# Kernel tuning notes

Hardware: AMD Instinct MI355X
Metric: run time of the kernel (lower is better)

The kernel has to match this reference:

```python
import jax, jax.numpy as jnp
import numpy as np

# static sizes
B, N_PER, D, H, L, DFF, IN_DIM = 32, 1024, 128, 4, 3, 2048, 64
N = B * N_PER
HD = D // H
EPS = 1e-5


def setup_inputs() -> dict:
    key = jax.random.key(0)
    ks = jax.random.split(key, 16)
    s = 0.02
    rn = lambda k, shp: jax.random.normal(k, shp, jnp.float32) * s
    return {
        "x": jax.random.normal(ks[0], (N, IN_DIM), jnp.float32),
        # uniform graph sizes -> static max_nodes; sorted graph ids
        "batch": jnp.repeat(jnp.arange(B, dtype=jnp.int32), N_PER),
        "W_in": rn(ks[1], (D, IN_DIM)),
        "b_in": rn(ks[2], (D,)),
        "Wqkv": rn(ks[3], (L, 3 * D, D)),
        "bqkv": rn(ks[4], (L, 3 * D)),
        "Wo": rn(ks[5], (L, D, D)),
        "bo": rn(ks[6], (L, D)),
        "W1": rn(ks[7], (L, DFF, D)),
        "b1": rn(ks[8], (L, DFF)),
        "W2": rn(ks[9], (L, D, DFF)),
        "b2": rn(ks[10], (L, D)),
        "ln1_g": jnp.ones((L, D), jnp.float32),
        "ln1_b": jnp.zeros((L, D), jnp.float32),
        "ln2_g": jnp.ones((L, D), jnp.float32),
        "ln2_b": jnp.zeros((L, D), jnp.float32),
    }


def _ln(x, g, b):
    m = x.mean(-1, keepdims=True)
    v = jnp.mean((x - m) ** 2, axis=-1, keepdims=True)
    return (x - m) / jnp.sqrt(v + EPS) * g + b


def _mha(h, Wqkv, bqkv, Wo, bo):
    # h: [B, S, D]
    qkv = h @ Wqkv.T + bqkv                      # [B, S, 3D]
    q, k, v = jnp.split(qkv, 3, axis=-1)
    q = q.reshape(B, -1, H, HD)
    k = k.reshape(B, -1, H, HD)
    v = v.reshape(B, -1, H, HD)
    att = jnp.einsum("bqhd,bkhd->bhqk", q, k) / np.sqrt(HD).astype(np.float32)
    p = jax.nn.softmax(att, axis=-1)
    o = jnp.einsum("bhqk,bkhd->bqhd", p, v).reshape(B, -1, D)
    return o @ Wo.T + bo


def reference(x, batch, W_in, b_in, Wqkv, bqkv, Wo, bo, W1, b1, W2, b2,
              ln1_g, ln1_b, ln2_g, ln2_b):
    # fused ragged -> padded: project all nodes once, scatter by (graph, pos)
    h = x @ W_in.T + b_in                        # [N, D]
    starts = jnp.searchsorted(batch, jnp.arange(B, dtype=batch.dtype))
    pos = jnp.arange(N, dtype=batch.dtype) - starts[batch]
    padded = jnp.zeros((B, N_PER, D), h.dtype).at[batch, pos].set(h)

    out = padded
    for l in range(L):  # post-LN TransformerEncoderLayer, dropout=eval
        a = _mha(out, Wqkv[l], bqkv[l], Wo[l], bo[l])
        out = _ln(out + a, ln1_g[l], ln1_b[l])
        f = jax.nn.relu(out @ W1[l].T + b1[l]) @ W2[l].T + b2[l]
        out = _ln(out + f, ln2_g[l], ln2_b[l])

    # mask derived from projected inputs, exactly as the original
    mask = (padded.sum(axis=2) != 0).astype(out.dtype)  # [B, S]
    return (out * mask[:, :, None]).sum(axis=1) / mask.sum(axis=1, keepdims=True)
```

## Files before the change

kernel.cpp:

```cpp
#include <hip/hip_runtime.h>
#include <hip/hip_bf16.h>
#include <stdint.h>

#define BB    32
#define NPER  1024
#define NTOT  32768
#define DD    128
#define HH    4
#define HD    32
#define LL    3
#define DFF   2048
#define INDIM 64
#define QKSCALE 0.17677669529663687f

typedef unsigned short u16;
typedef short bf16x8 __attribute__((ext_vector_type(8)));
typedef float f32x4 __attribute__((ext_vector_type(4)));

#define AS_GLOBAL(p) ((const __attribute__((address_space(1))) void*)(p))
#define AS_LDS(p)    ((__attribute__((address_space(3))) void*)(p))

__device__ __forceinline__ float bf2f(u16 v){
  unsigned u = ((unsigned)v) << 16; float f; __builtin_memcpy(&f, &u, 4); return f;
}
__device__ __forceinline__ u16 f2bf(float f){
  unsigned u; __builtin_memcpy(&u, &f, 4);
  unsigned lsb = (u >> 16) & 1u;
  u += 0x7fffu + lsb;
  return (u16)(u >> 16);
}

constexpr size_t OFF_FLAG   = 0;
constexpr size_t OFF_STARTS = 256;
constexpr size_t OFF_BIN    = 1024;
constexpr size_t OFF_BQKV   = OFF_BIN   + 128*4;
constexpr size_t OFF_BO     = OFF_BQKV  + 1152*4;
constexpr size_t OFF_B1     = OFF_BO    + 384*4;
constexpr size_t OFF_B2     = OFF_B1    + 6144*4;
constexpr size_t OFF_LN1G   = OFF_B2    + 384*4;
constexpr size_t OFF_LN1B   = OFF_LN1G  + 384*4;
constexpr size_t OFF_LN2G   = OFF_LN1B  + 384*4;
constexpr size_t OFF_LN2B   = OFF_LN2G  + 384*4;
constexpr size_t OFF_XB     = 40960;
constexpr size_t OFF_WINB   = OFF_XB    + (size_t)2097152*2;
constexpr size_t OFF_WQKVB  = OFF_WINB  + (size_t)8192*2;
constexpr size_t OFF_WOB    = OFF_WQKVB + (size_t)147456*2;
constexpr size_t OFF_W1B    = OFF_WOB   + (size_t)49152*2;
constexpr size_t OFF_W2B    = OFF_W1B   + (size_t)786432*2;
constexpr size_t OFF_CUR    = OFF_W2B   + (size_t)786432*2;
constexpr size_t OFF_TMP    = OFF_CUR   + (size_t)4194304*4;
constexpr size_t OFF_CURB   = OFF_TMP   + (size_t)4194304*4;
constexpr size_t OFF_QKVB   = OFF_CURB  + (size_t)4194304*2;
constexpr size_t OFF_ATTNOB = OFF_QKVB  + (size_t)12582912*2;
constexpr size_t OFF_ACTB   = OFF_ATTNOB+ (size_t)4194304*2;
constexpr size_t OFF_MASK   = OFF_ACTB  + (size_t)16777216*2;
constexpr size_t OFF_VT     = OFF_MASK  + (size_t)NTOT*4;
constexpr size_t OFF_RED    = OFF_VT    + (size_t)4096*1024*2;
constexpr size_t OFF_CNT    = OFF_RED   + (size_t)32*8*128*4;

__device__ __forceinline__ int plaus(unsigned bits){
  if ((bits << 1) == 0u) return 1;
  unsigned e = (bits >> 23) & 0xFFu;
  return (e >= 100u && e <= 140u) ? 1 : 0;
}
__global__ void detect_kernel(const unsigned* __restrict__ x, int* __restrict__ flag){
  __shared__ int red[256];
  int t = threadIdx.x, c = 0;
  for (int i = t; i < 2048; i += 256){
    unsigned w = x[i];
    c += (plaus(w << 16) & plaus(w & 0xFFFF0000u));
  }
  red[t] = c; __syncthreads();
  for (int s = 128; s > 0; s >>= 1){ if (t < s) red[t] += red[t+s]; __syncthreads(); }
  if (t == 0) *flag = (red[0] >= 1229) ? 1 : 0;
}

__global__ void starts_kernel(const int* __restrict__ batch, int* __restrict__ starts){
  int b = threadIdx.x;
  if (b < BB){
    int lo = 0, hi = NTOT;
    while (lo < hi){ int mid = (lo + hi) >> 1; if (batch[mid] < b) lo = mid + 1; else hi = mid; }
    starts[b] = lo;
  }
}

struct ConvSeg { const void* src; void* dst; int n; int tobf; };
struct ConvArgs { ConvSeg s[15]; };

__global__ __launch_bounds__(256) void convall_kernel(ConvArgs a, const int* __restrict__ flag){
  const int isb = *flag;
  const int blk = blockIdx.x;
  int seg = -1, base = 0, lb = 0;
  #pragma unroll
  for (int i = 0; i < 15; ++i){
    int nb = (a.s[i].n + 1023) >> 10;
    if (seg < 0){
      if (blk < base + nb){ seg = i; lb = blk - base; }
      base += nb;
    }
  }
  const ConvSeg sg = a.s[seg];
  const int idx = lb*1024 + threadIdx.x*4;
  if (idx >= sg.n) return;
  if (sg.tobf){
    u16* dst = (u16*)sg.dst + idx;
    if (isb){
      *(uint2*)dst = *(const uint2*)((const u16*)sg.src + idx);
    } else {
      const float* s4 = (const float*)sg.src + idx;
      dst[0] = f2bf(s4[0]); dst[1] = f2bf(s4[1]);
      dst[2] = f2bf(s4[2]); dst[3] = f2bf(s4[3]);
    }
  } else {
    float* dst = (float*)sg.dst + idx;
    if (isb){
      const u16* s4 = (const u16*)sg.src + idx;
      dst[0] = bf2f(s4[0]); dst[1] = bf2f(s4[1]);
      dst[2] = bf2f(s4[2]); dst[3] = bf2f(s4[3]);
    } else {
      *(float4*)dst = *(const float4*)((const float*)sg.src + idx);
    }
  }
}

__global__ __launch_bounds__(256) void gemm_bf16(
    const u16* __restrict__ A, int lda,
    const u16* __restrict__ W, int ldw,
    const float* __restrict__ bias,
    float* __restrict__ Cf, u16* __restrict__ Cb,
    int N, int K, int flags)
{
  __shared__ __align__(16) u16 At[64][32];
  __shared__ __align__(16) u16 Wt[64][32];
  const int t = threadIdx.x;
  const int m0 = blockIdx.x * 64, n0 = blockIdx.y * 64;
  const int wave = t >> 6, lane = t & 63;
  const int quad = lane >> 4, l16 = lane & 15;
  const int lr = t >> 2, lc = (t & 3) * 8;

  f32x4 acc[4];
  #pragma unroll
  for (int i = 0; i < 4; ++i){ acc[i][0]=0.f; acc[i][1]=0.f; acc[i][2]=0.f; acc[i][3]=0.f; }

  const u16* Arow = A + (size_t)(m0 + lr) * lda + lc;
  const u16* Wrow = W + (size_t)(n0 + lr) * ldw + lc;

  for (int k0 = 0; k0 < K; k0 += 32){
    uint4 av = *(const uint4*)(Arow + k0);
    uint4 wv = *(const uint4*)(Wrow + k0);
    __syncthreads();
    *(uint4*)&At[lr][lc] = av;
    *(uint4*)&Wt[lr][lc] = wv;
    __syncthreads();
    bf16x8 af = *(const bf16x8*)&At[wave*16 + l16][quad*8];
    #pragma unroll
    for (int nt = 0; nt < 4; ++nt){
      bf16x8 wf = *(const bf16x8*)&Wt[nt*16 + l16][quad*8];
      acc[nt] = __builtin_amdgcn_mfma_f32_16x16x32_bf16(af, wf, acc[nt], 0, 0, 0);
    }
  }
  const int row = m0 + wave*16 + quad*4;
  #pragma unroll
  for (int nt = 0; nt < 4; ++nt){
    const int col = n0 + nt*16 + l16;
    const float bv = bias ? bias[col] : 0.f;
    #pragma unroll
    for (int r = 0; r < 4; ++r){
      size_t idx = (size_t)(row + r) * N + col;
      float v = acc[nt][r] + bv;
      if (flags & 1) v = fmaxf(v, 0.f);
      if (Cf) Cf[idx] = v;
      if (Cb) Cb[idx] = f2bf(v);
    }
  }
}

__global__ __launch_bounds__(128) void scatter_kernel(
    const float* __restrict__ hlin, const int* __restrict__ batch,
    const int* __restrict__ starts, float* __restrict__ cur,
    u16* __restrict__ curb, float* __restrict__ mask)
{
  int i = blockIdx.x, t = threadIdx.x;
  int g = batch[i];
  int p = i - starts[g];
  float v = hlin[(size_t)i*DD + t];
  float s = v;
  #pragma unroll
  for (int off = 32; off; off >>= 1) s += __shfl_xor(s, off);
  __shared__ float sh[2];
  if ((t & 63) == 0) sh[t >> 6] = s;
  __syncthreads();
  float rowsum = sh[0] + sh[1];
  if ((unsigned)p < (unsigned)NPER && (unsigned)g < (unsigned)BB){
    size_t j = (size_t)g*NPER + p;
    cur[j*DD + t]  = v;
    curb[j*DD + t] = f2bf(v);
    if (t == 0) mask[j] = (rowsum != 0.f) ? 1.f : 0.f;
  }
}

__global__ __launch_bounds__(256) void fattn_kernel(
    const u16* __restrict__ qkvb,
    const u16* __restrict__ vt,
    u16* __restrict__ attnob)
{
  __shared__ __align__(16) u16 Klds[2][2048];
  __shared__ __align__(16) u16 Vl[2][2048];
  __shared__ __align__(16) u16 Pl[4][2][16*72];

  const int t = threadIdx.x;
  const int wave = t >> 6, lane = t & 63;
  const int quad = lane >> 4, l16 = lane & 15;
  const int q0 = blockIdx.x * 128;
  const int h = blockIdx.y, b = blockIdx.z;
  const size_t qkvbase = (size_t)b * NPER * 384;
  const u16* Kg = qkvb + qkvbase + 128 + h*HD;
  const u16* Vg = vt + (size_t)((b*HH + h)*HD) * NPER;

  bf16x8 qf[2];
  #pragma unroll
  for (int qt = 0; qt < 2; ++qt){
    const u16* qp = qkvb + qkvbase + (size_t)(q0 + wave*32 + qt*16 + l16)*384 + h*HD + quad*8;
    uint4 qv = *(const uint4*)qp;
    u16 raw[8]; __builtin_memcpy(raw, &qv, 16);
    #pragma unroll
    for (int j = 0; j < 8; ++j) qf[qt][j] = (short)f2bf(bf2f(raw[j]) * QKSCALE);
  }

  const int vcv = wave*2 + (lane >> 5), vd = lane & 31;
  auto stage = [&](int buf, int kt){
    __builtin_amdgcn_global_load_lds(
        AS_GLOBAL(Kg + (size_t)(kt*64 + lane)*384 + wave*8),
        AS_LDS(&Klds[buf][wave*64*8]), 16, 0, 0);
    __builtin_amdgcn_global_load_lds(
        AS_GLOBAL(Vg + (size_t)vd*NPER + kt*64 + vcv*8),
        AS_LDS(&Vl[buf][wave*64*8]), 16, 0, 0);
  };

  float lsum[2] = {0.f, 0.f};
  f32x4 o[2][2];
  #pragma unroll
  for (int qt = 0; qt < 2; ++qt)
    #pragma unroll
    for (int i = 0; i < 2; ++i){ o[qt][i][0]=0.f; o[qt][i][1]=0.f; o[qt][i][2]=0.f; o[qt][i][3]=0.f; }

  stage(0, 0);
  asm volatile("s_waitcnt vmcnt(0)" ::: "memory");
  __syncthreads();

  for (int kt = 0; kt < 16; ++kt){
    const int buf = kt & 1;
    if (kt + 1 < 16) stage(buf ^ 1, kt + 1);

    f32x4 sfr[2][4];
    #pragma unroll
    for (int nt = 0; nt < 4; ++nt){
      bf16x8 kf = *(const bf16x8*)&Klds[buf][(quad*64 + nt*16 + l16)*8];
      f32x4 z = {0.f,0.f,0.f,0.f};
      sfr[0][nt] = __builtin_amdgcn_mfma_f32_16x16x32_bf16(kf, qf[0], z, 0, 0, 0);
      sfr[1][nt] = __builtin_amdgcn_mfma_f32_16x16x32_bf16(kf, qf[1], z, 0, 0, 0);
    }

    #pragma unroll
    for (int qt = 0; qt < 2; ++qt){
      float ps = 0.f;
      #pragma unroll
      for (int nt = 0; nt < 4; ++nt){
        float e0 = __expf(sfr[qt][nt][0]), e1 = __expf(sfr[qt][nt][1]);
        float e2 = __expf(sfr[qt][nt][2]), e3 = __expf(sfr[qt][nt][3]);
        ps += (e0 + e1) + (e2 + e3);
        uint2 w;
        w.x = (unsigned)f2bf(e0) | ((unsigned)f2bf(e1) << 16);
        w.y = (unsigned)f2bf(e2) | ((unsigned)f2bf(e3) << 16);
        *(uint2*)&Pl[wave][qt][l16*72 + nt*16 + quad*4] = w;
      }
      ps += __shfl_xor(ps, 16);
      ps += __shfl_xor(ps, 32);
      lsum[qt] += ps;
    }
    asm volatile("s_waitcnt lgkmcnt(0)" ::: "memory");

    #pragma unroll
    for (int kk = 0; kk < 2; ++kk){
      bf16x8 v0 = *(const bf16x8*)&Vl[buf][((kk*4 + quad)*32 + l16)*8];
      bf16x8 v1 = *(const bf16x8*)&Vl[buf][((kk*4 + quad)*32 + 16 + l16)*8];
      #pragma unroll
      for (int qt = 0; qt < 2; ++qt){
        bf16x8 pf = *(const bf16x8*)&Pl[wave][qt][l16*72 + kk*32 + quad*8];
        o[qt][0] = __builtin_amdgcn_mfma_f32_16x16x32_bf16(pf, v0, o[qt][0], 0, 0, 0);
        o[qt][1] = __builtin_amdgcn_mfma_f32_16x16x32_bf16(pf, v1, o[qt][1], 0, 0, 0);
      }
    }

    if (kt + 1 < 16){
      asm volatile("s_waitcnt vmcnt(0)" ::: "memory");
      __syncthreads();
    }
  }

  #pragma unroll
  for (int qt = 0; qt < 2; ++qt){
    #pragma unroll
    for (int r = 0; r < 4; ++r){
      float inv = 1.f / __shfl(lsum[qt], quad*4 + r);
      int row = q0 + wave*32 + qt*16 + quad*4 + r;
      size_t base = (size_t)(b*NPER + row)*DD + h*HD;
      attnob[base + l16]      = f2bf(o[qt][0][r] * inv);
      attnob[base + 16 + l16] = f2bf(o[qt][1][r] * inv);
    }
  }
}

__device__ __forceinline__ void epilogue_ln64(
    const f32x4 O[8], int m0, int wave, int quad, int l16,
    const float* __restrict__ bias, const float* __restrict__ g,
    const float* __restrict__ beta, float* __restrict__ cur,
    u16* __restrict__ curb)
{
  #pragma unroll
  for (int rr = 0; rr < 4; ++rr){
    int row = m0 + wave*16 + quad*4 + rr;
    float vs[8], sum = 0.f;
    #pragma unroll
    for (int nt = 0; nt < 8; ++nt){
      int col = nt*16 + l16;
      float v = O[nt][rr] + bias[col] + cur[(size_t)row*DD + col];
      vs[nt] = v; sum += v;
    }
    sum += __shfl_xor(sum, 1); sum += __shfl_xor(sum, 2);
    sum += __shfl_xor(sum, 4); sum += __shfl_xor(sum, 8);
    float mean = sum * (1.f/DD);
    float sq = 0.f;
    #pragma unroll
    for (int nt = 0; nt < 8; ++nt){ float d = vs[nt] - mean; sq += d*d; }
    sq += __shfl_xor(sq, 1); sq += __shfl_xor(sq, 2);
    sq += __shfl_xor(sq, 4); sq += __shfl_xor(sq, 8);
    float rs = rsqrtf(sq * (1.f/DD) + 1e-5f);
    #pragma unroll
    for (int nt = 0; nt < 8; ++nt){
      int col = nt*16 + l16;
      float o = (vs[nt] - mean)*rs*g[col] + beta[col];
      cur[(size_t)row*DD + col]  = o;
      curb[(size_t)row*DD + col] = f2bf(o);
    }
  }
}

__global__ __launch_bounds__(256) void wgemm_kernel(
    const u16* __restrict__ A,
    const u16* __restrict__ Wbase,
    const float* __restrict__ biasb,
    int mode,
    u16* __restrict__ outb, int opitch,
    u16* __restrict__ vtout,
    float* __restrict__ cur, u16* __restrict__ curb,
    const float* __restrict__ g, const float* __restrict__ beta)
{
  __shared__ __align__(16) u16 Wl[16384];
  const int t = threadIdx.x, wave = t >> 6, lane = t & 63;
  const int quad = lane >> 4, l16 = lane & 15;
  const int m0 = blockIdx.x * 64, nb = blockIdx.y;
  const u16* Wsl = Wbase + (size_t)nb * 16384;
  const float* bias = biasb + nb * 128;

  #pragma unroll
  for (int j = 0; j < 8; ++j){
    int s = t + 256*j;
    int r = s >> 4, cx = (s & 15) ^ (r & 15);
    *(uint4*)&Wl[s*8] = *(const uint4*)(Wsl + (size_t)r*128 + cx*8);
  }
  bf16x8 af[4];
  #pragma unroll
  for (int kk = 0; kk < 4; ++kk)
    af[kk] = *(const bf16x8*)(A + (size_t)(m0 + wave*16 + l16)*128 + kk*32 + quad*8);
  __syncthreads();

  f32x4 O[8];
  #pragma unroll
  for (int nt = 0; nt < 8; ++nt){ O[nt][0]=0.f; O[nt][1]=0.f; O[nt][2]=0.f; O[nt][3]=0.f; }

  #pragma unroll
  for (int nt = 0; nt < 8; ++nt){
    int row = nt*16 + l16;
    bf16x8 wf[4];
    #pragma unroll
    for (int kk = 0; kk < 4; ++kk)
      wf[kk] = *(const bf16x8*)&Wl[(row*16 + ((kk*4 + quad) ^ l16))*8];
    #pragma unroll
    for (int kk = 0; kk < 4; ++kk)
      O[nt] = __builtin_amdgcn_mfma_f32_16x16x32_bf16(af[kk], wf[kk], O[nt], 0, 0, 0);
  }

  if (mode == 0){
    if (nb == 2 && vtout){
      int rowb = m0 + wave*16 + quad*4;
      int bg = rowb >> 10, s = rowb & 1023;
      #pragma unroll
      for (int nt = 0; nt < 8; ++nt){
        int col = nt*16 + l16;
        int hh = col >> 5, d = col & 31;
        float v0 = O[nt][0] + bias[col], v1 = O[nt][1] + bias[col];
        float v2 = O[nt][2] + bias[col], v3 = O[nt][3] + bias[col];
        uint2 w;
        w.x = (unsigned)f2bf(v0) | ((unsigned)f2bf(v1) << 16);
        w.y = (unsigned)f2bf(v2) | ((unsigned)f2bf(v3) << 16);
        *(uint2*)(vtout + (size_t)((bg*HH + hh)*HD + d)*NPER + s) = w;
      }
    } else {
      #pragma unroll
      for (int rr = 0; rr < 4; ++rr){
        int row = m0 + wave*16 + quad*4 + rr;
        #pragma unroll
        for (int nt = 0; nt < 8; ++nt){
          int col = nt*16 + l16;
          outb[(size_t)row*opitch + nb*128 + col] = f2bf(O[nt][rr] + bias[col]);
        }
      }
    }
  } else {
    epilogue_ln64(O, m0, wave, quad, l16, bias, g, beta, cur, curb);
  }
}

__global__ __launch_bounds__(256, 2) void ffn_kernel(
    const u16* __restrict__ Ag,
    const u16* __restrict__ W1g,
    const u16* __restrict__ W2g,
    const float* __restrict__ b1,
    const float* __restrict__ b2,
    const float* __restrict__ g, const float* __restrict__ beta,
    float* __restrict__ cur, u16* __restrict__ curb)
{
  __shared__ __align__(16) u16 W1l[2][8192];
  __shared__ __align__(16) u16 W2l[2][8192];
  __shared__ __align__(16) u16 Pl[4][16*72];

  const int t = threadIdx.x, wave = t >> 6, lane = t & 63;
  const int quad = lane >> 4, l16 = lane & 15;
  const int m0 = blockIdx.x * 64;
  u16* Pw = &Pl[wave][0];

  auto stage = [&](int buf, int dffc){
    #pragma unroll
    for (int i = 0; i < 4; ++i){
      const int s0 = wave*256 + i*64;
      const int s  = s0 + lane;
      { int r = s >> 4, cx = (s & 15) ^ (r & 15);
        __builtin_amdgcn_global_load_lds(
            AS_GLOBAL(W1g + (size_t)(dffc + r)*128 + cx*8),
            AS_LDS(&W1l[buf][s0*8]), 16, 0, 0); }
      { int r = s >> 3, cx = (s & 7) ^ (r & 7);
        __builtin_amdgcn_global_load_lds(
            AS_GLOBAL(W2g + (size_t)r*DFF + dffc + cx*8),
            AS_LDS(&W2l[buf][s0*8]), 16, 0, 0); }
    }
  };

  bf16x8 af[4];
  #pragma unroll
  for (int kk = 0; kk < 4; ++kk)
    af[kk] = *(const bf16x8*)(Ag + (size_t)(m0 + wave*16 + l16)*128 + kk*32 + quad*8);

  f32x4 O[8];
  #pragma unroll
  for (int nt = 0; nt < 8; ++nt){ O[nt][0]=0.f; O[nt][1]=0.f; O[nt][2]=0.f; O[nt][3]=0.f; }

  stage(0, 0);
  asm volatile("s_waitcnt vmcnt(0)" ::: "memory");
  __syncthreads();

  for (int c = 0; c < 32; ++c){
    const int buf = c & 1;
    if (c + 1 < 32) stage(buf ^ 1, (c + 1)*64);

    #pragma unroll
    for (int nt = 0; nt < 4; ++nt){
      int row = nt*16 + l16;
      bf16x8 wf[4];
      #pragma unroll
      for (int kk = 0; kk < 4; ++kk)
        wf[kk] = *(const bf16x8*)&W1l[buf][(row*16 + ((kk*4 + quad) ^ l16))*8];
      f32x4 b1v = *(const f32x4*)&b1[c*64 + nt*16 + quad*4];
      f32x4 s = {0.f,0.f,0.f,0.f};
      #pragma unroll
      for (int kk = 0; kk < 4; ++kk)
        s = __builtin_amdgcn_mfma_f32_16x16x32_bf16(wf[kk], af[kk], s, 0, 0, 0);
      float v0 = fmaxf(s[0] + b1v[0], 0.f), v1 = fmaxf(s[1] + b1v[1], 0.f);
      float v2 = fmaxf(s[2] + b1v[2], 0.f), v3 = fmaxf(s[3] + b1v[3], 0.f);
      uint2 w;
      w.x = (unsigned)f2bf(v0) | ((unsigned)f2bf(v1) << 16);
      w.y = (unsigned)f2bf(v2) | ((unsigned)f2bf(v3) << 16);
      *(uint2*)&Pw[l16*72 + nt*16 + quad*4] = w;
    }
    asm volatile("s_waitcnt lgkmcnt(0)" ::: "memory");

    bf16x8 pf[2];
    #pragma unroll
    for (int kk = 0; kk < 2; ++kk)
      pf[kk] = *(const bf16x8*)&Pw[l16*72 + kk*32 + quad*8];
    #pragma unroll
    for (int nt = 0; nt < 8; ++nt){
      int row = nt*16 + l16;
      bf16x8 wf[2];
      #pragma unroll
      for (int kk = 0; kk < 2; ++kk)
        wf[kk] = *(const bf16x8*)&W2l[buf][(row*8 + ((kk*4 + quad) ^ (l16 & 7)))*8];
      #pragma unroll
      for (int kk = 0; kk < 2; ++kk)
        O[nt] = __builtin_amdgcn_mfma_f32_16x16x32_bf16(pf[kk], wf[kk], O[nt], 0, 0, 0);
    }

    if (c + 1 < 32){
      asm volatile("s_waitcnt vmcnt(0)" ::: "memory");
      __syncthreads();
    }
  }

  epilogue_ln64(O, m0, wave, quad, l16, b2, g, beta, cur, curb);
}

__global__ __launch_bounds__(128) void reduce1_kernel(
    const float* __restrict__ cur, const float* __restrict__ mask,
    float* __restrict__ partial, float* __restrict__ cnt)
{
  int b = blockIdx.x, c = blockIdx.y, t = threadIdx.x;
  float acc = 0.f, cn = 0.f;
  for (int s = c*128; s < c*128 + 128; ++s){
    float mk = mask[b*NPER + s];
    acc += cur[(size_t)(b*NPER + s)*DD + t] * mk;
    cn += mk;
  }
  partial[(size_t)(b*8 + c)*DD + t] = acc;
  if (t == 0) cnt[b*8 + c] = cn;
}
__global__ __launch_bounds__(128) void reduce2_kernel(
    const float* __restrict__ partial, const float* __restrict__ cnt,
    const int* __restrict__ flag, void* __restrict__ out)
{
  int b = blockIdx.x, t = threadIdx.x;
  float acc = 0.f, cn = 0.f;
  #pragma unroll
  for (int c = 0; c < 8; ++c){
    acc += partial[(size_t)(b*8 + c)*DD + t];
    cn  += cnt[b*8 + c];
  }
  float val = acc / cn;
  if (*flag) ((u16*)out)[b*DD + t] = f2bf(val);
  else       ((float*)out)[b*DD + t] = val;
}

extern "C" void kernel_launch(void* const* d_in, const int* in_sizes, int n_in,
                              void* d_out, int out_size, void* d_ws, size_t ws_size,
                              hipStream_t stream)
{
  (void)in_sizes; (void)n_in; (void)out_size; (void)ws_size;
  char* ws = (char*)d_ws;
  int*   flag   = (int*)(ws + OFF_FLAG);
  int*   starts = (int*)(ws + OFF_STARTS);
  float* BIN  = (float*)(ws + OFF_BIN);
  float* BQKV = (float*)(ws + OFF_BQKV);
  float* BO   = (float*)(ws + OFF_BO);
  float* B1   = (float*)(ws + OFF_B1);
  float* B2   = (float*)(ws + OFF_B2);
  float* LN1G = (float*)(ws + OFF_LN1G);
  float* LN1B = (float*)(ws + OFF_LN1B);
  float* LN2G = (float*)(ws + OFF_LN2G);
  float* LN2B = (float*)(ws + OFF_LN2B);
  u16* XB    = (u16*)(ws + OFF_XB);
  u16* WINB  = (u16*)(ws + OFF_WINB);
  u16* WQKVB = (u16*)(ws + OFF_WQKVB);
  u16* WOB   = (u16*)(ws + OFF_WOB);
  u16* W1B   = (u16*)(ws + OFF_W1B);
  u16* W2B   = (u16*)(ws + OFF_W2B);
  float* CUR = (float*)(ws + OFF_CUR);
  float* TMP = (float*)(ws + OFF_TMP);
  u16* CURB  = (u16*)(ws + OFF_CURB);
  u16* QKVB  = (u16*)(ws + OFF_QKVB);
  u16* ATTNOB= (u16*)(ws + OFF_ATTNOB);
  float* MASK= (float*)(ws + OFF_MASK);
  u16* VT    = (u16*)(ws + OFF_VT);
  float* RED = (float*)(ws + OFF_RED);
  float* CNT = (float*)(ws + OFF_CNT);

  detect_kernel<<<1, 256, 0, stream>>>((const unsigned*)d_in[0], flag);
  starts_kernel<<<1, 64, 0, stream>>>((const int*)d_in[1], starts);

  ConvArgs ca;
  ca.s[0]  = { d_in[0],  XB,    NTOT*INDIM, 1 };
  ca.s[1]  = { d_in[2],  WINB,  DD*INDIM,   1 };
  ca.s[2]  = { d_in[4],  WQKVB, LL*3*DD*DD, 1 };
  ca.s[3]  = { d_in[6],  WOB,   LL*DD*DD,   1 };
  ca.s[4]  = { d_in[8],  W1B,   LL*DFF*DD,  1 };
  ca.s[5]  = { d_in[10], W2B,   LL*DD*DFF,  1 };
  ca.s[6]  = { d_in[3],  BIN,   DD,         0 };
  ca.s[7]  = { d_in[5],  BQKV,  LL*3*DD,    0 };
  ca.s[8]  = { d_in[7],  BO,    LL*DD,      0 };
  ca.s[9]  = { d_in[9],  B1,    LL*DFF,     0 };
  ca.s[10] = { d_in[11], B2,    LL*DD,      0 };
  ca.s[11] = { d_in[12], LN1G,  LL*DD,      0 };
  ca.s[12] = { d_in[13], LN1B,  LL*DD,      0 };
  ca.s[13] = { d_in[14], LN2G,  LL*DD,      0 };
  ca.s[14] = { d_in[15], LN2B,  LL*DD,      0 };
  int nblk = 0;
  for (int i = 0; i < 15; ++i) nblk += (ca.s[i].n + 1023) >> 10;
  convall_kernel<<<nblk, 256, 0, stream>>>(ca, flag);

  gemm_bf16<<<dim3(NTOT/64, DD/64), 256, 0, stream>>>(
      XB, INDIM, WINB, INDIM, BIN, TMP, nullptr, DD, INDIM, 0);
  scatter_kernel<<<NTOT, 128, 0, stream>>>(TMP, (const int*)d_in[1], starts, CUR, CURB, MASK);

  for (int l = 0; l < LL; ++l){
    wgemm_kernel<<<dim3(NTOT/64, 3), 256, 0, stream>>>(
        CURB, WQKVB + (size_t)l*3*DD*DD, BQKV + l*3*DD, 0,
        QKVB, 384, VT, nullptr, nullptr, nullptr, nullptr);
    fattn_kernel<<<dim3(NPER/128, HH, BB), 256, 0, stream>>>(QKVB, VT, ATTNOB);
    wgemm_kernel<<<dim3(NTOT/64, 1), 256, 0, stream>>>(
        ATTNOB, WOB + (size_t)l*DD*DD, BO + l*DD, 1,
        nullptr, 0, nullptr, CUR, CURB, LN1G + l*DD, LN1B + l*DD);
    ffn_kernel<<<dim3(NTOT/64), 256, 0, stream>>>(
        CURB, W1B + (size_t)l*DFF*DD, W2B + (size_t)l*DD*DFF,
        B1 + l*DFF, B2 + l*DD, LN2G + l*DD, LN2B + l*DD, CUR, CURB);
  }

  reduce1_kernel<<<dim3(BB, 8), 128, 0, stream>>>(CUR, MASK, RED, CNT);
  reduce2_kernel<<<BB, 128, 0, stream>>>(RED, CNT, flag, d_out);
}
```

Baseline: 507.8 us.

## Fuse input projection with scatter, widen QKV GEMM tile, restructure FFN P store

```diff
diff --git a/kernel.cpp b/kernel.cpp
--- a/kernel.cpp
+++ b/kernel.cpp
@@ -123,79 +123,69 @@
   }
 }
 
-__global__ __launch_bounds__(256) void gemm_bf16(
-    const u16* __restrict__ A, int lda,
-    const u16* __restrict__ W, int ldw,
-    const float* __restrict__ bias,
-    float* __restrict__ Cf, u16* __restrict__ Cb,
-    int N, int K, int flags)
-{
-  __shared__ __align__(16) u16 At[64][32];
-  __shared__ __align__(16) u16 Wt[64][32];
-  const int t = threadIdx.x;
-  const int m0 = blockIdx.x * 64, n0 = blockIdx.y * 64;
-  const int wave = t >> 6, lane = t & 63;
+__global__ __launch_bounds__(256) void inproj_kernel(
+    const u16* __restrict__ XB,
+    const u16* __restrict__ WINB,
+    const float* __restrict__ bin,
+    const int* __restrict__ batch, const int* __restrict__ starts,
+    float* __restrict__ cur, u16* __restrict__ curb, float* __restrict__ mask)
+{
+  __shared__ __align__(16) u16 Wl[8192];
+  const int t = threadIdx.x, wave = t >> 6, lane = t & 63;
   const int quad = lane >> 4, l16 = lane & 15;
-  const int lr = t >> 2, lc = (t & 3) * 8;
-
-  f32x4 acc[4];
-  #pragma unroll
-  for (int i = 0; i < 4; ++i){ acc[i][0]=0.f; acc[i][1]=0.f; acc[i][2]=0.f; acc[i][3]=0.f; }
-
-  const u16* Arow = A + (size_t)(m0 + lr) * lda + lc;
-  const u16* Wrow = W + (size_t)(n0 + lr) * ldw + lc;
-
-  for (int k0 = 0; k0 < K; k0 += 32){
-    uint4 av = *(const uint4*)(Arow + k0);
-    uint4 wv = *(const uint4*)(Wrow + k0);
-    __syncthreads();
-    *(uint4*)&At[lr][lc] = av;
-    *(uint4*)&Wt[lr][lc] = wv;
-    __syncthreads();
-    bf16x8 af = *(const bf16x8*)&At[wave*16 + l16][quad*8];
-    #pragma unroll
-    for (int nt = 0; nt < 4; ++nt){
-      bf16x8 wf = *(const bf16x8*)&Wt[nt*16 + l16][quad*8];
-      acc[nt] = __builtin_amdgcn_mfma_f32_16x16x32_bf16(af, wf, acc[nt], 0, 0, 0);
-    }
-  }
-  const int row = m0 + wave*16 + quad*4;
-  #pragma unroll
-  for (int nt = 0; nt < 4; ++nt){
-    const int col = n0 + nt*16 + l16;
-    const float bv = bias ? bias[col] : 0.f;
-    #pragma unroll
-    for (int r = 0; r < 4; ++r){
-      size_t idx = (size_t)(row + r) * N + col;
-      float v = acc[nt][r] + bv;
-      if (flags & 1) v = fmaxf(v, 0.f);
-      if (Cf) Cf[idx] = v;
-      if (Cb) Cb[idx] = f2bf(v);
-    }
-  }
-}
-
-__global__ __launch_bounds__(128) void scatter_kernel(
-    const float* __restrict__ hlin, const int* __restrict__ batch,
-    const int* __restrict__ starts, float* __restrict__ cur,
-    u16* __restrict__ curb, float* __restrict__ mask)
-{
-  int i = blockIdx.x, t = threadIdx.x;
-  int g = batch[i];
-  int p = i - starts[g];
-  float v = hlin[(size_t)i*DD + t];
-  float s = v;
-  #pragma unroll
-  for (int off = 32; off; off >>= 1) s += __shfl_xor(s, off);
-  __shared__ float sh[2];
-  if ((t & 63) == 0) sh[t >> 6] = s;
+  const int m0 = blockIdx.x * 64;
+
+  #pragma unroll
+  for (int j = 0; j < 4; ++j){
+    int s = t + 256*j;
+    int r = s >> 3, c8 = (s & 7) ^ (r & 7);
+    *(uint4*)&Wl[s*8] = *(const uint4*)(WINB + (size_t)r*INDIM + c8*8);
+  }
+  bf16x8 af[2];
+  #pragma unroll
+  for (int kk = 0; kk < 2; ++kk)
+    af[kk] = *(const bf16x8*)(XB + (size_t)(m0 + wave*16 + l16)*INDIM + kk*32 + quad*8);
   __syncthreads();
-  float rowsum = sh[0] + sh[1];
-  if ((unsigned)p < (unsigned)NPER && (unsigned)g < (unsigned)BB){
-    size_t j = (size_t)g*NPER + p;
-    cur[j*DD + t]  = v;
-    curb[j*DD + t] = f2bf(v);
-    if (t == 0) mask[j] = (rowsum != 0.f) ? 1.f : 0.f;
+
+  f32x4 O[8];
+  #pragma unroll
+  for (int nt = 0; nt < 8; ++nt){ O[nt][0]=0.f; O[nt][1]=0.f; O[nt][2]=0.f; O[nt][3]=0.f; }
+
+  #pragma unroll
+  for (int nt = 0; nt < 8; ++nt){
+    int row = nt*16 + l16;
+    bf16x8 wf[2];
+    #pragma unroll
+    for (int kk = 0; kk < 2; ++kk)
+      wf[kk] = *(const bf16x8*)&Wl[(row*8 + ((kk*4 + quad) ^ (row & 7)))*8];
+    #pragma unroll
+    for (int kk = 0; kk < 2; ++kk)
+      O[nt] = __builtin_amdgcn_mfma_f32_16x16x32_bf16(af[kk], wf[kk], O[nt], 0, 0, 0);
+  }
+
+  #pragma unroll
+  for (int rr = 0; rr < 4; ++rr){
+    int node = m0 + wave*16 + quad*4 + rr;
+    int gr = batch[node];
+    int p  = node - starts[gr];
+    float vs[8], sum = 0.f;
+    #pragma unroll
+    for (int nt = 0; nt < 8; ++nt){
+      float v = O[nt][rr] + bin[nt*16 + l16];
+      vs[nt] = v; sum += v;
+    }
+    sum += __shfl_xor(sum, 1); sum += __shfl_xor(sum, 2);
+    sum += __shfl_xor(sum, 4); sum += __shfl_xor(sum, 8);
+    if ((unsigned)p < (unsigned)NPER && (unsigned)gr < (unsigned)BB){
+      size_t j = (size_t)gr*NPER + p;
+      #pragma unroll
+      for (int nt = 0; nt < 8; ++nt){
+        int col = nt*16 + l16;
+        cur[j*DD + col]  = vs[nt];
+        curb[j*DD + col] = f2bf(vs[nt]);
+      }
+      if (l16 == 0) mask[j] = (sum != 0.f) ? 1.f : 0.f;
+    }
   }
 }
 
@@ -350,16 +340,56 @@
     const u16* __restrict__ A,
     const u16* __restrict__ Wbase,
     const float* __restrict__ biasb,
-    int mode,
-    u16* __restrict__ outb, int opitch,
-    u16* __restrict__ vtout,
     float* __restrict__ cur, u16* __restrict__ curb,
     const float* __restrict__ g, const float* __restrict__ beta)
 {
   __shared__ __align__(16) u16 Wl[16384];
   const int t = threadIdx.x, wave = t >> 6, lane = t & 63;
   const int quad = lane >> 4, l16 = lane & 15;
-  const int m0 = blockIdx.x * 64, nb = blockIdx.y;
+  const int m0 = blockIdx.x * 64;
+
+  #pragma unroll
+  for (int j = 0; j < 8; ++j){
+    int s = t + 256*j;
+    int r = s >> 4, cx = (s & 15) ^ (r & 15);
+    *(uint4*)&Wl[s*8] = *(const uint4*)(Wbase + (size_t)r*128 + cx*8);
+  }
+  bf16x8 af[4];
+  #pragma unroll
+  for (int kk = 0; kk < 4; ++kk)
+    af[kk] = *(const bf16x8*)(A + (size_t)(m0 + wave*16 + l16)*128 + kk*32 + quad*8);
+  __syncthreads();
+
+  f32x4 O[8];
+  #pragma unroll
+  for (int nt = 0; nt < 8; ++nt){ O[nt][0]=0.f; O[nt][1]=0.f; O[nt][2]=0.f; O[nt][3]=0.f; }
+
+  #pragma unroll
+  for (int nt = 0; nt < 8; ++nt){
+    int row = nt*16 + l16;
+    bf16x8 wf[4];
+    #pragma unroll
+    for (int kk = 0; kk < 4; ++kk)
+      wf[kk] = *(const bf16x8*)&Wl[(row*16 + ((kk*4 + quad) ^ l16))*8];
+    #pragma unroll
+    for (int kk = 0; kk < 4; ++kk)
+      O[nt] = __builtin_amdgcn_mfma_f32_16x16x32_bf16(af[kk], wf[kk], O[nt], 0, 0, 0);
+  }
+
+  epilogue_ln64(O, m0, wave, quad, l16, biasb, g, beta, cur, curb);
+}
+
+__global__ __launch_bounds__(256) void wgemm2_kernel(
+    const u16* __restrict__ A,
+    const u16* __restrict__ Wbase,
+    const float* __restrict__ biasb,
+    u16* __restrict__ outb, int opitch,
+    u16* __restrict__ vtout)
+{
+  __shared__ __align__(16) u16 Wl[16384];
+  const int t = threadIdx.x, wave = t >> 6, lane = t & 63;
+  const int quad = lane >> 4, l16 = lane & 15;
+  const int m0 = blockIdx.x * 128, nb = blockIdx.y;
   const u16* Wsl = Wbase + (size_t)nb * 16384;
   const float* bias = biasb + nb * 128;
 
@@ -369,15 +399,19 @@
     int r = s >> 4, cx = (s & 15) ^ (r & 15);
     *(uint4*)&Wl[s*8] = *(const uint4*)(Wsl + (size_t)r*128 + cx*8);
   }
-  bf16x8 af[4];
-  #pragma unroll
-  for (int kk = 0; kk < 4; ++kk)
-    af[kk] = *(const bf16x8*)(A + (size_t)(m0 + wave*16 + l16)*128 + kk*32 + quad*8);
+  bf16x8 af[2][4];
+  #pragma unroll
+  for (int mt = 0; mt < 2; ++mt)
+    #pragma unroll
+    for (int kk = 0; kk < 4; ++kk)
+      af[mt][kk] = *(const bf16x8*)(A + (size_t)(m0 + wave*32 + mt*16 + l16)*128 + kk*32 + quad*8);
   __syncthreads();
 
-  f32x4 O[8];
-  #pragma unroll
-  for (int nt = 0; nt < 8; ++nt){ O[nt][0]=0.f; O[nt][1]=0.f; O[nt][2]=0.f; O[nt][3]=0.f; }
+  f32x4 O[2][8];
+  #pragma unroll
+  for (int mt = 0; mt < 2; ++mt)
+    #pragma unroll
+    for (int nt = 0; nt < 8; ++nt){ O[mt][nt][0]=0.f; O[mt][nt][1]=0.f; O[mt][nt][2]=0.f; O[mt][nt][3]=0.f; }
 
   #pragma unroll
   for (int nt = 0; nt < 8; ++nt){
@@ -387,38 +421,41 @@
     for (int kk = 0; kk < 4; ++kk)
       wf[kk] = *(const bf16x8*)&Wl[(row*16 + ((kk*4 + quad) ^ l16))*8];
     #pragma unroll
-    for (int kk = 0; kk < 4; ++kk)
-      O[nt] = __builtin_amdgcn_mfma_f32_16x16x32_bf16(af[kk], wf[kk], O[nt], 0, 0, 0);
-  }
-
-  if (mode == 0){
-    if (nb == 2 && vtout){
-      int rowb = m0 + wave*16 + quad*4;
+    for (int mt = 0; mt < 2; ++mt)
+      #pragma unroll
+      for (int kk = 0; kk < 4; ++kk)
+        O[mt][nt] = __builtin_amdgcn_mfma_f32_16x16x32_bf16(af[mt][kk], wf[kk], O[mt][nt], 0, 0, 0);
+  }
+
+  if (nb == 2){
+    #pragma unroll
+    for (int mt = 0; mt < 2; ++mt){
+      int rowb = m0 + wave*32 + mt*16 + quad*4;
       int bg = rowb >> 10, s = rowb & 1023;
       #pragma unroll
       for (int nt = 0; nt < 8; ++nt){
         int col = nt*16 + l16;
         int hh = col >> 5, d = col & 31;
-        float v0 = O[nt][0] + bias[col], v1 = O[nt][1] + bias[col];
-        float v2 = O[nt][2] + bias[col], v3 = O[nt][3] + bias[col];
+        float v0 = O[mt][nt][0] + bias[col], v1 = O[mt][nt][1] + bias[col];
+        float v2 = O[mt][nt][2] + bias[col], v3 = O[mt][nt][3] + bias[col];
         uint2 w;
         w.x = (unsigned)f2bf(v0) | ((unsigned)f2bf(v1) << 16);
         w.y = (unsigned)f2bf(v2) | ((unsigned)f2bf(v3) << 16);
         *(uint2*)(vtout + (size_t)((bg*HH + hh)*HD + d)*NPER + s) = w;
       }
-    } else {
+    }
+  } else {
+    #pragma unroll
+    for (int mt = 0; mt < 2; ++mt)
       #pragma unroll
       for (int rr = 0; rr < 4; ++rr){
-        int row = m0 + wave*16 + quad*4 + rr;
+        int row = m0 + wave*32 + mt*16 + quad*4 + rr;
         #pragma unroll
         for (int nt = 0; nt < 8; ++nt){
           int col = nt*16 + l16;
-          outb[(size_t)row*opitch + nb*128 + col] = f2bf(O[nt][rr] + bias[col]);
+          outb[(size_t)row*opitch + nb*128 + col] = f2bf(O[mt][nt][rr] + bias[col]);
         }
       }
-    }
-  } else {
-    epilogue_ln64(O, m0, wave, quad, l16, bias, g, beta, cur, curb);
   }
 }
 
@@ -480,17 +517,14 @@
       #pragma unroll
       for (int kk = 0; kk < 4; ++kk)
         wf[kk] = *(const bf16x8*)&W1l[buf][(row*16 + ((kk*4 + quad) ^ l16))*8];
-      f32x4 b1v = *(const f32x4*)&b1[c*64 + nt*16 + quad*4];
+      float b1v = b1[c*64 + row];
       f32x4 s = {0.f,0.f,0.f,0.f};
       #pragma unroll
       for (int kk = 0; kk < 4; ++kk)
-        s = __builtin_amdgcn_mfma_f32_16x16x32_bf16(wf[kk], af[kk], s, 0, 0, 0);
-      float v0 = fmaxf(s[0] + b1v[0], 0.f), v1 = fmaxf(s[1] + b1v[1], 0.f);
-      float v2 = fmaxf(s[2] + b1v[2], 0.f), v3 = fmaxf(s[3] + b1v[3], 0.f);
-      uint2 w;
-      w.x = (unsigned)f2bf(v0) | ((unsigned)f2bf(v1) << 16);
-      w.y = (unsigned)f2bf(v2) | ((unsigned)f2bf(v3) << 16);
-      *(uint2*)&Pw[l16*72 + nt*16 + quad*4] = w;
+        s = __builtin_amdgcn_mfma_f32_16x16x32_bf16(af[kk], wf[kk], s, 0, 0, 0);
+      #pragma unroll
+      for (int rr = 0; rr < 4; ++rr)
+        Pw[(quad*4 + rr)*72 + nt*16 + l16] = f2bf(fmaxf(s[rr] + b1v, 0.f));
     }
     asm volatile("s_waitcnt lgkmcnt(0)" ::: "memory");
 
@@ -573,7 +607,6 @@
   u16* W1B   = (u16*)(ws + OFF_W1B);
   u16* W2B   = (u16*)(ws + OFF_W2B);
   float* CUR = (float*)(ws + OFF_CUR);
-  float* TMP = (float*)(ws + OFF_TMP);
   u16* CURB  = (u16*)(ws + OFF_CURB);
   u16* QKVB  = (u16*)(ws + OFF_QKVB);
   u16* ATTNOB= (u16*)(ws + OFF_ATTNOB);
@@ -605,18 +638,15 @@
   for (int i = 0; i < 15; ++i) nblk += (ca.s[i].n + 1023) >> 10;
   convall_kernel<<<nblk, 256, 0, stream>>>(ca, flag);
 
-  gemm_bf16<<<dim3(NTOT/64, DD/64), 256, 0, stream>>>(
-      XB, INDIM, WINB, INDIM, BIN, TMP, nullptr, DD, INDIM, 0);
-  scatter_kernel<<<NTOT, 128, 0, stream>>>(TMP, (const int*)d_in[1], starts, CUR, CURB, MASK);
+  inproj_kernel<<<NTOT/64, 256, 0, stream>>>(
+      XB, WINB, BIN, (const int*)d_in[1], starts, CUR, CURB, MASK);
 
   for (int l = 0; l < LL; ++l){
-    wgemm_kernel<<<dim3(NTOT/64, 3), 256, 0, stream>>>(
-        CURB, WQKVB + (size_t)l*3*DD*DD, BQKV + l*3*DD, 0,
-        QKVB, 384, VT, nullptr, nullptr, nullptr, nullptr);
+    wgemm2_kernel<<<dim3(NTOT/128, 3), 256, 0, stream>>>(
+        CURB, WQKVB + (size_t)l*3*DD*DD, BQKV + l*3*DD, QKVB, 384, VT);
     fattn_kernel<<<dim3(NPER/128, HH, BB), 256, 0, stream>>>(QKVB, VT, ATTNOB);
-    wgemm_kernel<<<dim3(NTOT/64, 1), 256, 0, stream>>>(
-        ATTNOB, WOB + (size_t)l*DD*DD, BO + l*DD, 1,
-        nullptr, 0, nullptr, CUR, CURB, LN1G + l*DD, LN1B + l*DD);
+    wgemm_kernel<<<dim3(NTOT/64), 256, 0, stream>>>(
+        ATTNOB, WOB + (size_t)l*DD*DD, BO + l*DD, CUR, CURB, LN1G + l*DD, LN1B + l*DD);
     ffn_kernel<<<dim3(NTOT/64), 256, 0, stream>>>(
         CURB, W1B + (size_t)l*DFF*DD, W2B + (size_t)l*DD*DFF,
         B1 + l*DFF, B2 + l*DD, LN2G + l*DD, LN2B + l*DD, CUR, CURB);
```

Result: faster. 493.3 us (-2.8%).
